# Kernel tuning notes

Measured on AMD Instinct MI355X. Metric: run time of the kernel, lower is better.

## Reference

```python
import jax, jax.numpy as jnp
import numpy as np

WH, WW = 7, 7
N = WH * WW
H = 16          # num_heads
D = 32          # head_dim
NW = 64         # num windows per image (mask.shape[0])


def _relative_position_index(wh, ww):
    coords = np.stack(np.meshgrid(np.arange(wh), np.arange(ww), indexing='ij'))  # (2, wh, ww)
    cf = coords.reshape(2, -1)                                                   # (2, N)
    rel = cf[:, :, None] - cf[:, None, :]                                        # (2, N, N)
    rel = rel.transpose(1, 2, 0).copy()
    rel[:, :, 0] += wh - 1
    rel[:, :, 1] += ww - 1
    rel[:, :, 0] *= 2 * ww - 1
    return rel.sum(-1)  # (N, N) int

REL_IDX = jnp.asarray(_relative_position_index(WH, WW))


def setup_inputs() -> dict:
    key = jax.random.key(0)
    ks = jax.random.split(key, 5)
    B_ = 2048
    dim = H * D
    x = jax.random.normal(ks[0], (B_, N, dim), dtype=jnp.float32)
    mask = jnp.zeros((NW, N, N), dtype=jnp.float32)
    rpb_table = jax.random.normal(ks[1], ((2 * WH - 1) * (2 * WW - 1), H), dtype=jnp.float32) * 0.02
    qkv_w = jax.random.normal(ks[2], (3 * dim, dim), dtype=jnp.float32) * (dim ** -0.5)
    qkv_b = jnp.zeros((3 * dim,), dtype=jnp.float32)
    proj_w = jax.random.normal(ks[3], (dim, dim), dtype=jnp.float32) * (dim ** -0.5)
    proj_b = jnp.zeros((dim,), dtype=jnp.float32)
    return {"x": x, "mask": mask, "rpb_table": rpb_table,
            "qkv_w": qkv_w, "qkv_b": qkv_b, "proj_w": proj_w, "proj_b": proj_b}


def reference(x, mask, rpb_table, qkv_w, qkv_b, proj_w, proj_b):
    B_, n, C = x.shape
    scale = D ** -0.5
    # qkv projection (torch Linear: x @ W^T + b)
    qkv = (x @ qkv_w.T + qkv_b).reshape(B_, n, 3, H, D)
    q = qkv[:, :, 0].transpose(0, 2, 1, 3) * scale  # (B_, H, N, D)
    k = qkv[:, :, 1].transpose(0, 2, 1, 3)
    v = qkv[:, :, 2].transpose(0, 2, 1, 3)
    attn = jnp.einsum('bhnd,bhmd->bhnm', q, k)      # (B_, H, N, N)
    # relative position bias: gather (N*N,) rows from table -> (N, N, H) -> (H, N, N)
    bias = rpb_table[REL_IDX.reshape(-1)].reshape(n, n, H).transpose(2, 0, 1)
    attn = attn + bias[None]
    # shifted-window mask add: (B, nW, H, N, N) + (1, nW, 1, N, N)
    nW = mask.shape[0]
    attn = attn.reshape(B_ // nW, nW, H, n, n) + mask[None, :, None]
    attn = attn.reshape(B_, H, n, n)
    attn = jax.nn.softmax(attn, axis=-1)
    out = jnp.einsum('bhnm,bhmd->bhnd', attn, v)    # (B_, H, N, D)
    out = out.transpose(0, 2, 1, 3).reshape(B_, n, H * D)
    return out @ proj_w.T + proj_b
```

## Files before the change

### kernel.cpp

```cpp
#include <hip/hip_runtime.h>

typedef _Float16 f16;
typedef _Float16 f16x8 __attribute__((ext_vector_type(8)));
typedef _Float16 f16x4 __attribute__((ext_vector_type(4)));
typedef float f32x4 __attribute__((ext_vector_type(4)));

#define NTOK 49
#define NH 16
#define HD 32
#define DIM 512
#define NWIN 64
#define NB 2048
#define MTOT (NB*NTOK)
#define SCALE 0.17677669529663687f
#define VTS 56

__device__ __forceinline__ void gload_lds16(const f16* g, f16* l) {
    __builtin_amdgcn_global_load_lds((const __attribute__((address_space(1))) void*)g,
                                     (__attribute__((address_space(3))) void*)l, 16, 0, 0);
}

__global__ __launch_bounds__(256) void cvt_f32_f16(const float* __restrict__ s,
                                                   f16* __restrict__ d, int n4) {
    int i = blockIdx.x * 256 + threadIdx.x;
    int st = gridDim.x * 256;
    for (; i < n4; i += st) {
        float4 v = ((const float4*)s)[i];
        f16x4 o = { (f16)v.x, (f16)v.y, (f16)v.z, (f16)v.w };
        *(f16x4*)(d + (size_t)i * 4) = o;
    }
}

__global__ __launch_bounds__(256) void build_comb2(const float* __restrict__ rpb,
                                                   const float* __restrict__ mask,
                                                   float* __restrict__ comb2) {
    int idx = blockIdx.x * 256 + threadIdx.x;
    int r4   = idx & 3;
    int tj   = (idx >> 2) & 3;
    int ti   = (idx >> 4) & 3;
    int lane = (idx >> 6) & 63;
    int wh   = idx >> 12;
    int h = wh & 15, w = wh >> 4;
    int g = lane >> 4, c16 = lane & 15;
    int row = ti * 16 + g * 4 + r4;
    int col = tj * 16 + c16;
    float v = 0.f;
    if (row < NTOK && col < NTOK) {
        int ri = row / 7, ci = row - ri * 7;
        int rj = col / 7, cj = col - rj * 7;
        int rel = (ri - rj + 6) * 13 + (ci - cj + 6);
        v = rpb[rel * NH + h] + mask[(w * NTOK + row) * NTOK + col];
    }
    comb2[idx] = v;
}

template<int MODE, int NT>
__global__ __launch_bounds__(256) void gemm_kernel(const f16* __restrict__ A,
                                                   const f16* __restrict__ Bw,
                                                   const float* __restrict__ bias,
                                                   f16* __restrict__ qo,
                                                   f16* __restrict__ ko,
                                                   f16* __restrict__ vto,
                                                   float* __restrict__ outp) {
    __shared__ __align__(16) f16 As[128][64];
    __shared__ __align__(16) f16 Bs[128][64];

    const int tid = threadIdx.x;
    const int lane = tid & 63;
    const int wv = tid >> 6;
    const int wr = wv >> 1, wc = wv & 1;
    const int g = lane >> 4, c16 = lane & 15;

    const int nblk = gridDim.x;
    const int f = blockIdx.x;
    const int work = (f & 7) * (nblk >> 3) + (f >> 3);
    const int m0 = (work / NT) * 128;
    const int n0 = (work % NT) * 128;

    const int sr8 = lane >> 3;
    const int scs = ((lane & 7) ^ sr8) * 8;
    const f16* gA = A + (size_t)(m0 + wv * 32 + sr8) * DIM + scs;
    const f16* gB = Bw + (size_t)(n0 + wv * 32 + sr8) * DIM + scs;

    f32x4 acc[4][4];
#pragma unroll
    for (int i = 0; i < 4; ++i)
#pragma unroll
        for (int j = 0; j < 4; ++j)
            acc[i][j] = (f32x4){0.f, 0.f, 0.f, 0.f};

    const int KS = DIM / 64;
    for (int ks = 0; ks < KS; ++ks) {
        const int k0 = ks * 64;
        __syncthreads();
#pragma unroll
        for (int i = 0; i < 4; ++i) {
            gload_lds16(gA + (size_t)(i * 8) * DIM + k0, &As[wv * 32 + i * 8][0]);
            gload_lds16(gB + (size_t)(i * 8) * DIM + k0, &Bs[wv * 32 + i * 8][0]);
        }
        __syncthreads();
#pragma unroll
        for (int kk = 0; kk < 2; ++kk) {
            f16x8 af[4], bf[4];
#pragma unroll
            for (int t = 0; t < 4; ++t)
                af[t] = *(const f16x8*)&As[wr * 64 + t * 16 + c16][((kk * 4 + g) ^ (c16 & 7)) * 8];
#pragma unroll
            for (int t = 0; t < 4; ++t)
                bf[t] = *(const f16x8*)&Bs[wc * 64 + t * 16 + c16][((kk * 4 + g) ^ (c16 & 7)) * 8];
            __builtin_amdgcn_s_setprio(1);
#pragma unroll
            for (int i = 0; i < 4; ++i)
#pragma unroll
                for (int j = 0; j < 4; ++j)
                    acc[i][j] = __builtin_amdgcn_mfma_f32_16x16x32_f16(af[i], bf[j], acc[i][j], 0, 0, 0);
            __builtin_amdgcn_s_setprio(0);
        }
    }

#pragma unroll
    for (int i = 0; i < 4; ++i)
#pragma unroll
        for (int r = 0; r < 4; ++r) {
            int m = m0 + wr * 64 + i * 16 + g * 4 + r;
            int b = 0, t = 0;
            if (MODE == 0) { b = m / NTOK; t = m - b * NTOK; }
#pragma unroll
            for (int j = 0; j < 4; ++j) {
                int n = n0 + wc * 64 + j * 16 + c16;
                float v = acc[i][j][r] + bias[n];
                if (MODE == 0) {
                    int s = n >> 9;
                    int hh = (n >> 5) & 15;
                    int d = n & 31;
                    int bh = b * NH + hh;
                    if (s == 0)      qo[((size_t)bh * NTOK + t) * HD + d] = (f16)(v * SCALE);
                    else if (s == 1) ko[((size_t)bh * NTOK + t) * HD + d] = (f16)v;
                    else             vto[((size_t)bh * HD + d) * VTS + t] = (f16)v;
                } else {
                    outp[(size_t)m * DIM + n] = v;
                }
            }
        }
}

__global__ __launch_bounds__(256) void attn_kernel(const f16* __restrict__ qw,
                                                   const f16* __restrict__ kw,
                                                   const f16* __restrict__ vt,
                                                   const float* __restrict__ comb2,
                                                   f16* __restrict__ aout) {
    __shared__ __align__(16) f16 Ps[4][64][72];

    const int wv = threadIdx.x >> 6;
    const int l = threadIdx.x & 63;
    const int f = blockIdx.x;
    const int work = (f & 7) * (gridDim.x >> 3) + (f >> 3);
    const int bid = work * 4 + wv;
    const int b = bid >> 4, h = bid & 15;
    const int w = b & (NWIN - 1);
    const int g = l >> 4, c16 = l & 15;
    const size_t qkbase = (size_t)bid * (NTOK * HD);
    const size_t vbase = (size_t)bid * (HD * VTS);

    const f16x8 z8 = {};

    f16x8 qf[4], kf[4];
#pragma unroll
    for (int t = 0; t < 4; ++t) {
        int row = t * 16 + c16;
        f16x8 q = z8, k = z8;
        if (row < NTOK) {
            q = *(const f16x8*)(qw + qkbase + row * HD + g * 8);
            k = *(const f16x8*)(kw + qkbase + row * HD + g * 8);
        }
        qf[t] = q; kf[t] = k;
    }

    const float* cb = comb2 + (((size_t)(w * NH + h) * 64 + l) << 6);
    f32x4 S[4][4];
#pragma unroll
    for (int i = 0; i < 4; ++i)
#pragma unroll
        for (int j = 0; j < 4; ++j)
            S[i][j] = *(const f32x4*)(cb + (i * 4 + j) * 4);
#pragma unroll
    for (int i = 0; i < 4; ++i)
#pragma unroll
        for (int j = 0; j < 4; ++j)
            S[i][j] = __builtin_amdgcn_mfma_f32_16x16x32_f16(qf[i], kf[j], S[i][j], 0, 0, 0);

#pragma unroll
    for (int ti = 0; ti < 4; ++ti)
#pragma unroll
        for (int r = 0; r < 4; ++r) {
            int row = ti * 16 + g * 4 + r;
            float v0 = S[ti][0][r], v1 = S[ti][1][r], v2 = S[ti][2][r];
            float v3 = (c16 == 0) ? S[ti][3][r] : -1e30f;
            float mx = fmaxf(fmaxf(v0, v1), fmaxf(v2, v3));
#pragma unroll
            for (int mk = 1; mk < 16; mk <<= 1) mx = fmaxf(mx, __shfl_xor(mx, mk, 64));
            float p0 = __expf(v0 - mx), p1 = __expf(v1 - mx), p2 = __expf(v2 - mx);
            float p3 = (c16 == 0) ? __expf(v3 - mx) : 0.f;
            float sm = p0 + p1 + p2 + p3;
#pragma unroll
            for (int mk = 1; mk < 16; mk <<= 1) sm += __shfl_xor(sm, mk, 64);
            float inv = 1.f / sm;
            Ps[wv][row][c16]      = (f16)(p0 * inv);
            Ps[wv][row][16 + c16] = (f16)(p1 * inv);
            Ps[wv][row][32 + c16] = (f16)(p2 * inv);
            Ps[wv][row][48 + c16] = (f16)(p3 * inv);
        }
    __syncthreads();

    f32x4 O[4][2];
    const f32x4 zf = (f32x4){0.f, 0.f, 0.f, 0.f};
#pragma unroll
    for (int i = 0; i < 4; ++i) { O[i][0] = zf; O[i][1] = zf; }
#pragma unroll
    for (int c = 0; c < 2; ++c) {
        f16x8 pf[4], vf[2];
#pragma unroll
        for (int ti = 0; ti < 4; ++ti)
            pf[ti] = *(const f16x8*)&Ps[wv][ti * 16 + c16][c * 32 + g * 8];
        int tcol = c * 32 + g * 8;
#pragma unroll
        for (int td = 0; td < 2; ++td) {
            f16x8 vv = z8;
            if (tcol < VTS)
                vv = *(const f16x8*)(vt + vbase + (size_t)(td * 16 + c16) * VTS + tcol);
            vf[td] = vv;
        }
#pragma unroll
        for (int ti = 0; ti < 4; ++ti)
#pragma unroll
            for (int td = 0; td < 2; ++td)
                O[ti][td] = __builtin_amdgcn_mfma_f32_16x16x32_f16(pf[ti], vf[td], O[ti][td], 0, 0, 0);
    }

#pragma unroll
    for (int ti = 0; ti < 4; ++ti)
#pragma unroll
        for (int r = 0; r < 4; ++r) {
            int row = ti * 16 + g * 4 + r;
            if (row < NTOK) {
                size_t ob = ((size_t)(b * NTOK + row)) * DIM + h * HD;
                aout[ob + c16]      = (f16)O[ti][0][r];
                aout[ob + 16 + c16] = (f16)O[ti][1][r];
            }
        }
}

extern "C" void kernel_launch(void* const* d_in, const int* in_sizes, int n_in,
                              void* d_out, int out_size, void* d_ws, size_t ws_size,
                              hipStream_t stream) {
    const float* x      = (const float*)d_in[0];
    const float* mask   = (const float*)d_in[1];
    const float* rpb    = (const float*)d_in[2];
    const float* qkv_w  = (const float*)d_in[3];
    const float* qkv_b  = (const float*)d_in[4];
    const float* proj_w = (const float*)d_in[5];
    const float* proj_b = (const float*)d_in[6];
    float* out = (float*)d_out;

    char* ws = (char*)d_ws;
    size_t o = 0;
    f16* x16   = (f16*)(ws + o); o += (size_t)MTOT * DIM * 2;
    f16* w16   = (f16*)(ws + o); o += (size_t)1536 * 512 * 2;
    f16* pw16  = (f16*)(ws + o); o += (size_t)512 * 512 * 2;
    f16* qws   = (f16*)(ws + o); o += (size_t)NB * NH * NTOK * HD * 2;
    f16* kws   = (f16*)(ws + o); o += (size_t)NB * NH * NTOK * HD * 2;
    f16* vtws  = (f16*)(ws + o); o += (size_t)NB * NH * HD * VTS * 2;
    float* cb2 = (float*)(ws + o);
    f16* aout = x16;

    cvt_f32_f16<<<dim3(2048), dim3(256), 0, stream>>>(x, x16, MTOT * DIM / 4);
    cvt_f32_f16<<<dim3(768), dim3(256), 0, stream>>>(qkv_w, w16, 1536 * 512 / 4);
    cvt_f32_f16<<<dim3(256), dim3(256), 0, stream>>>(proj_w, pw16, 512 * 512 / 4);

    build_comb2<<<dim3(16384), dim3(256), 0, stream>>>(rpb, mask, cb2);

    gemm_kernel<0, 12><<<dim3((MTOT / 128) * 12), dim3(256), 0, stream>>>(
        x16, w16, qkv_b, qws, kws, vtws, nullptr);

    attn_kernel<<<dim3(NB * NH / 4), dim3(256), 0, stream>>>(qws, kws, vtws, cb2, aout);

    gemm_kernel<1, 4><<<dim3((MTOT / 128) * 4), dim3(256), 0, stream>>>(
        aout, pw16, proj_b, nullptr, nullptr, nullptr, out);
}
```

Before: 658.5 us.

## Switch GEMMs to 256x256 tiles with double-buffered LDS prefetch

```diff
diff --git a/kernel.cpp b/kernel.cpp
--- a/kernel.cpp
+++ b/kernel.cpp
@@ -55,79 +55,139 @@
 }
 
 template<int MODE, int NT>
-__global__ __launch_bounds__(256) void gemm_kernel(const f16* __restrict__ A,
-                                                   const f16* __restrict__ Bw,
-                                                   const float* __restrict__ bias,
-                                                   f16* __restrict__ qo,
-                                                   f16* __restrict__ ko,
-                                                   f16* __restrict__ vto,
-                                                   float* __restrict__ outp) {
-    __shared__ __align__(16) f16 As[128][64];
-    __shared__ __align__(16) f16 Bs[128][64];
+__global__ __launch_bounds__(512, 2) void gemm256(const f16* __restrict__ A,
+                                                  const f16* __restrict__ Bw,
+                                                  const float* __restrict__ bias,
+                                                  f16* __restrict__ qo,
+                                                  f16* __restrict__ ko,
+                                                  f16* __restrict__ vto,
+                                                  float* __restrict__ outp) {
+    __shared__ __align__(16) f16 As[2][256][64];
+    __shared__ __align__(16) f16 Bs[2][256][64];
 
     const int tid = threadIdx.x;
     const int lane = tid & 63;
     const int wv = tid >> 6;
-    const int wr = wv >> 1, wc = wv & 1;
+    const int wm = wv >> 2, wn = wv & 3;
     const int g = lane >> 4, c16 = lane & 15;
+    const int sl8 = lane >> 3;
+    const int sc8 = (lane & 7) ^ sl8;
 
     const int nblk = gridDim.x;
     const int f = blockIdx.x;
     const int work = (f & 7) * (nblk >> 3) + (f >> 3);
-    const int m0 = (work / NT) * 128;
-    const int n0 = (work % NT) * 128;
-
-    const int sr8 = lane >> 3;
-    const int scs = ((lane & 7) ^ sr8) * 8;
-    const f16* gA = A + (size_t)(m0 + wv * 32 + sr8) * DIM + scs;
-    const f16* gB = Bw + (size_t)(n0 + wv * 32 + sr8) * DIM + scs;
-
-    f32x4 acc[4][4];
-#pragma unroll
-    for (int i = 0; i < 4; ++i)
+    const int m0 = (work / NT) * 256;
+    const int n0 = (work % NT) * 256;
+
+    const f16* gA0 = A  + (size_t)(m0 + wv * 8 + sl8) * DIM + sc8 * 8;
+    const f16* gB0 = Bw + (size_t)(n0 + wv * 8 + sl8) * DIM + sc8 * 8;
+
+#define STAGE(buf, kof, rd) \
+    gload_lds16(gA0 + (size_t)((rd) * 64) * DIM + (kof), &As[buf][(rd) * 64 + wv * 8][0]); \
+    gload_lds16(gB0 + (size_t)((rd) * 64) * DIM + (kof), &Bs[buf][(rd) * 64 + wv * 8][0]);
+
+#define ARD(half, t2, kk) (*(const f16x8*)&As[pb][wm * 128 + (half) * 64 + (t2) * 16 + c16][((((kk) * 4 + g)) ^ (c16 & 7)) * 8])
+#define BRD(half, j2, kk) (*(const f16x8*)&Bs[pb][wn * 64 + (half) * 32 + (j2) * 16 + c16][((((kk) * 4 + g)) ^ (c16 & 7)) * 8])
+
+    f32x4 acc[8][4];
+#pragma unroll
+    for (int i = 0; i < 8; ++i)
 #pragma unroll
         for (int j = 0; j < 4; ++j)
             acc[i][j] = (f32x4){0.f, 0.f, 0.f, 0.f};
 
-    const int KS = DIM / 64;
-    for (int ks = 0; ks < KS; ++ks) {
-        const int k0 = ks * 64;
-        __syncthreads();
-#pragma unroll
-        for (int i = 0; i < 4; ++i) {
-            gload_lds16(gA + (size_t)(i * 8) * DIM + k0, &As[wv * 32 + i * 8][0]);
-            gload_lds16(gB + (size_t)(i * 8) * DIM + k0, &Bs[wv * 32 + i * 8][0]);
-        }
-        __syncthreads();
-#pragma unroll
-        for (int kk = 0; kk < 2; ++kk) {
-            f16x8 af[4], bf[4];
-#pragma unroll
-            for (int t = 0; t < 4; ++t)
-                af[t] = *(const f16x8*)&As[wr * 64 + t * 16 + c16][((kk * 4 + g) ^ (c16 & 7)) * 8];
-#pragma unroll
-            for (int t = 0; t < 4; ++t)
-                bf[t] = *(const f16x8*)&Bs[wc * 64 + t * 16 + c16][((kk * 4 + g) ^ (c16 & 7)) * 8];
-            __builtin_amdgcn_s_setprio(1);
-#pragma unroll
-            for (int i = 0; i < 4; ++i)
-#pragma unroll
-                for (int j = 0; j < 4; ++j)
-                    acc[i][j] = __builtin_amdgcn_mfma_f32_16x16x32_f16(af[i], bf[j], acc[i][j], 0, 0, 0);
-            __builtin_amdgcn_s_setprio(0);
-        }
-    }
-
-#pragma unroll
-    for (int i = 0; i < 4; ++i)
+#pragma unroll
+    for (int rd = 0; rd < 4; ++rd) { STAGE(0, 0, rd) }
+    asm volatile("s_waitcnt vmcnt(0)" ::: "memory");
+    __builtin_amdgcn_s_barrier();
+
+    const int KT = DIM / 64;
+    for (int t = 0; t < KT; ++t) {
+        const int pb = t & 1, nb = pb ^ 1;
+        const int kn = (t + 1) * 64;
+        const bool hasn = (t + 1 < KT);
+        f16x8 af0[4][2], af1[4][2], bf0[2][2], bf1[2][2];
+
+#pragma unroll
+        for (int t2 = 0; t2 < 4; ++t2)
+#pragma unroll
+            for (int kk = 0; kk < 2; ++kk) af0[t2][kk] = ARD(0, t2, kk);
+#pragma unroll
+        for (int j2 = 0; j2 < 2; ++j2)
+#pragma unroll
+            for (int kk = 0; kk < 2; ++kk) bf0[j2][kk] = BRD(0, j2, kk);
+        if (hasn) { STAGE(nb, kn, 0) STAGE(nb, kn, 1) }
+        __builtin_amdgcn_s_barrier();
+        __builtin_amdgcn_s_setprio(1);
+#pragma unroll
+        for (int t2 = 0; t2 < 4; ++t2)
+#pragma unroll
+            for (int j2 = 0; j2 < 2; ++j2)
+#pragma unroll
+                for (int kk = 0; kk < 2; ++kk)
+                    acc[t2][j2] = __builtin_amdgcn_mfma_f32_16x16x32_f16(af0[t2][kk], bf0[j2][kk], acc[t2][j2], 0, 0, 0);
+        __builtin_amdgcn_s_setprio(0);
+        __builtin_amdgcn_s_barrier();
+
+#pragma unroll
+        for (int j2 = 0; j2 < 2; ++j2)
+#pragma unroll
+            for (int kk = 0; kk < 2; ++kk) bf1[j2][kk] = BRD(1, j2, kk);
+        if (hasn) { STAGE(nb, kn, 2) STAGE(nb, kn, 3) }
+        __builtin_amdgcn_s_barrier();
+        __builtin_amdgcn_s_setprio(1);
+#pragma unroll
+        for (int t2 = 0; t2 < 4; ++t2)
+#pragma unroll
+            for (int j2 = 0; j2 < 2; ++j2)
+#pragma unroll
+                for (int kk = 0; kk < 2; ++kk)
+                    acc[t2][2 + j2] = __builtin_amdgcn_mfma_f32_16x16x32_f16(af0[t2][kk], bf1[j2][kk], acc[t2][2 + j2], 0, 0, 0);
+        __builtin_amdgcn_s_setprio(0);
+        __builtin_amdgcn_s_barrier();
+
+#pragma unroll
+        for (int t2 = 0; t2 < 4; ++t2)
+#pragma unroll
+            for (int kk = 0; kk < 2; ++kk) af1[t2][kk] = ARD(1, t2, kk);
+        __builtin_amdgcn_s_barrier();
+        __builtin_amdgcn_s_setprio(1);
+#pragma unroll
+        for (int t2 = 0; t2 < 4; ++t2)
+#pragma unroll
+            for (int j2 = 0; j2 < 2; ++j2)
+#pragma unroll
+                for (int kk = 0; kk < 2; ++kk)
+                    acc[4 + t2][j2] = __builtin_amdgcn_mfma_f32_16x16x32_f16(af1[t2][kk], bf0[j2][kk], acc[4 + t2][j2], 0, 0, 0);
+        __builtin_amdgcn_s_setprio(0);
+        __builtin_amdgcn_s_barrier();
+
+        __builtin_amdgcn_s_setprio(1);
+#pragma unroll
+        for (int t2 = 0; t2 < 4; ++t2)
+#pragma unroll
+            for (int j2 = 0; j2 < 2; ++j2)
+#pragma unroll
+                for (int kk = 0; kk < 2; ++kk)
+                    acc[4 + t2][2 + j2] = __builtin_amdgcn_mfma_f32_16x16x32_f16(af1[t2][kk], bf1[j2][kk], acc[4 + t2][2 + j2], 0, 0, 0);
+        __builtin_amdgcn_s_setprio(0);
+        if (hasn) asm volatile("s_waitcnt vmcnt(0)" ::: "memory");
+        __builtin_amdgcn_s_barrier();
+    }
+#undef STAGE
+#undef ARD
+#undef BRD
+
+#pragma unroll
+    for (int i = 0; i < 8; ++i)
 #pragma unroll
         for (int r = 0; r < 4; ++r) {
-            int m = m0 + wr * 64 + i * 16 + g * 4 + r;
+            int m = m0 + wm * 128 + i * 16 + g * 4 + r;
             int b = 0, t = 0;
             if (MODE == 0) { b = m / NTOK; t = m - b * NTOK; }
 #pragma unroll
             for (int j = 0; j < 4; ++j) {
-                int n = n0 + wc * 64 + j * 16 + c16;
+                int n = n0 + wn * 64 + j * 16 + c16;
                 float v = acc[i][j][r] + bias[n];
                 if (MODE == 0) {
                     int s = n >> 9;
@@ -279,11 +339,11 @@
 
     build_comb2<<<dim3(16384), dim3(256), 0, stream>>>(rpb, mask, cb2);
 
-    gemm_kernel<0, 12><<<dim3((MTOT / 128) * 12), dim3(256), 0, stream>>>(
+    gemm256<0, 6><<<dim3((MTOT / 256) * 6), dim3(512), 0, stream>>>(
         x16, w16, qkv_b, qws, kws, vtws, nullptr);
 
     attn_kernel<<<dim3(NB * NH / 4), dim3(256), 0, stream>>>(qws, kws, vtws, cb2, aout);
 
-    gemm_kernel<1, 4><<<dim3((MTOT / 128) * 4), dim3(256), 0, stream>>>(
+    gemm256<1, 2><<<dim3((MTOT / 256) * 2), dim3(512), 0, stream>>>(
         aout, pw16, proj_b, nullptr, nullptr, nullptr, out);
 }
```

Result: slower. 692.6 us (+5.2%).

## Triple-buffer GEMM K-loop with async LDS loads and vectorized transposed epilogue

Applied to the files above, without the earlier changes.

```diff
diff --git a/kernel.cpp b/kernel.cpp
--- a/kernel.cpp
+++ b/kernel.cpp
@@ -55,21 +55,22 @@
 }
 
 template<int MODE, int NT>
-__global__ __launch_bounds__(256) void gemm_kernel(const f16* __restrict__ A,
-                                                   const f16* __restrict__ Bw,
-                                                   const float* __restrict__ bias,
-                                                   f16* __restrict__ qo,
-                                                   f16* __restrict__ ko,
-                                                   f16* __restrict__ vto,
-                                                   float* __restrict__ outp) {
-    __shared__ __align__(16) f16 As[128][64];
-    __shared__ __align__(16) f16 Bs[128][64];
+__global__ __launch_bounds__(256, 3) void gemm_kernel(const f16* __restrict__ A,
+                                                      const f16* __restrict__ Bw,
+                                                      const float* __restrict__ bias,
+                                                      f16* __restrict__ qo,
+                                                      f16* __restrict__ ko,
+                                                      f16* __restrict__ vto,
+                                                      float* __restrict__ outp) {
+    __shared__ __align__(16) f16 As[3][128][32];
+    __shared__ __align__(16) f16 Bs[3][128][32];
 
     const int tid = threadIdx.x;
     const int lane = tid & 63;
     const int wv = tid >> 6;
     const int wr = wv >> 1, wc = wv & 1;
     const int g = lane >> 4, c16 = lane & 15;
+    const int rsw = (c16 >> 1) & 3;
 
     const int nblk = gridDim.x;
     const int f = blockIdx.x;
@@ -77,71 +78,94 @@
     const int m0 = (work / NT) * 128;
     const int n0 = (work % NT) * 128;
 
-    const int sr8 = lane >> 3;
-    const int scs = ((lane & 7) ^ sr8) * 8;
-    const f16* gA = A + (size_t)(m0 + wv * 32 + sr8) * DIM + scs;
-    const f16* gB = Bw + (size_t)(n0 + wv * 32 + sr8) * DIM + scs;
+    const int srow = lane >> 2;
+    const int schunk = (lane & 3) ^ ((srow >> 1) & 3);
+    const f16* gA = A  + (size_t)(m0 + wv * 32 + srow) * DIM + schunk * 8;
+    const f16* gB = Bw + (size_t)(n0 + wv * 32 + srow) * DIM + schunk * 8;
+
+#define STAGE(buf, t) do { \
+    gload_lds16(gA + (t) * 32,                     &As[buf][wv * 32][0]);      \
+    gload_lds16(gA + (size_t)16 * DIM + (t) * 32,  &As[buf][wv * 32 + 16][0]); \
+    gload_lds16(gB + (t) * 32,                     &Bs[buf][wv * 32][0]);      \
+    gload_lds16(gB + (size_t)16 * DIM + (t) * 32,  &Bs[buf][wv * 32 + 16][0]); \
+} while (0)
 
     f32x4 acc[4][4];
 #pragma unroll
-    for (int i = 0; i < 4; ++i)
+    for (int j = 0; j < 4; ++j)
+#pragma unroll
+        for (int i = 0; i < 4; ++i)
+            acc[j][i] = (f32x4){0.f, 0.f, 0.f, 0.f};
+
+    STAGE(0, 0);
+    STAGE(1, 1);
+    asm volatile("s_waitcnt vmcnt(4)" ::: "memory");
+    __builtin_amdgcn_s_barrier();
+
+    const int KS = DIM / 32;
+#pragma unroll
+    for (int t = 0; t < KS; ++t) {
+        const int cb = t % 3;
+        if (t + 2 < KS) STAGE((t + 2) % 3, t + 2);
+        f16x8 af[4], bf[4];
+#pragma unroll
+        for (int i = 0; i < 4; ++i)
+            af[i] = *(const f16x8*)&As[cb][wr * 64 + i * 16 + c16][(g ^ rsw) * 8];
 #pragma unroll
         for (int j = 0; j < 4; ++j)
-            acc[i][j] = (f32x4){0.f, 0.f, 0.f, 0.f};
-
-    const int KS = DIM / 64;
-    for (int ks = 0; ks < KS; ++ks) {
-        const int k0 = ks * 64;
-        __syncthreads();
-#pragma unroll
-        for (int i = 0; i < 4; ++i) {
-            gload_lds16(gA + (size_t)(i * 8) * DIM + k0, &As[wv * 32 + i * 8][0]);
-            gload_lds16(gB + (size_t)(i * 8) * DIM + k0, &Bs[wv * 32 + i * 8][0]);
-        }
-        __syncthreads();
-#pragma unroll
-        for (int kk = 0; kk < 2; ++kk) {
-            f16x8 af[4], bf[4];
-#pragma unroll
-            for (int t = 0; t < 4; ++t)
-                af[t] = *(const f16x8*)&As[wr * 64 + t * 16 + c16][((kk * 4 + g) ^ (c16 & 7)) * 8];
-#pragma unroll
-            for (int t = 0; t < 4; ++t)
-                bf[t] = *(const f16x8*)&Bs[wc * 64 + t * 16 + c16][((kk * 4 + g) ^ (c16 & 7)) * 8];
-            __builtin_amdgcn_s_setprio(1);
+            bf[j] = *(const f16x8*)&Bs[cb][wc * 64 + j * 16 + c16][(g ^ rsw) * 8];
+        __builtin_amdgcn_s_setprio(1);
+#pragma unroll
+        for (int j = 0; j < 4; ++j)
 #pragma unroll
             for (int i = 0; i < 4; ++i)
-#pragma unroll
-                for (int j = 0; j < 4; ++j)
-                    acc[i][j] = __builtin_amdgcn_mfma_f32_16x16x32_f16(af[i], bf[j], acc[i][j], 0, 0, 0);
-            __builtin_amdgcn_s_setprio(0);
-        }
-    }
-
-#pragma unroll
-    for (int i = 0; i < 4; ++i)
-#pragma unroll
-        for (int r = 0; r < 4; ++r) {
-            int m = m0 + wr * 64 + i * 16 + g * 4 + r;
-            int b = 0, t = 0;
-            if (MODE == 0) { b = m / NTOK; t = m - b * NTOK; }
-#pragma unroll
-            for (int j = 0; j < 4; ++j) {
-                int n = n0 + wc * 64 + j * 16 + c16;
-                float v = acc[i][j][r] + bias[n];
-                if (MODE == 0) {
-                    int s = n >> 9;
-                    int hh = (n >> 5) & 15;
-                    int d = n & 31;
-                    int bh = b * NH + hh;
-                    if (s == 0)      qo[((size_t)bh * NTOK + t) * HD + d] = (f16)(v * SCALE);
-                    else if (s == 1) ko[((size_t)bh * NTOK + t) * HD + d] = (f16)v;
-                    else             vto[((size_t)bh * HD + d) * VTS + t] = (f16)v;
+                acc[j][i] = __builtin_amdgcn_mfma_f32_16x16x32_f16(bf[j], af[i], acc[j][i], 0, 0, 0);
+        __builtin_amdgcn_s_setprio(0);
+        asm volatile("s_waitcnt lgkmcnt(0)" ::: "memory");
+        __builtin_amdgcn_sched_barrier(0);
+        if (t + 2 < KS) {
+            asm volatile("s_waitcnt vmcnt(4)" ::: "memory");
+        } else if (t + 1 < KS) {
+            asm volatile("s_waitcnt vmcnt(0)" ::: "memory");
+        }
+        if (t + 1 < KS) __builtin_amdgcn_s_barrier();
+    }
+#undef STAGE
+
+#pragma unroll
+    for (int i = 0; i < 4; ++i) {
+        const int m = m0 + wr * 64 + i * 16 + c16;
+        int b = 0, tk = 0;
+        if (MODE == 0) { b = m / NTOK; tk = m - b * NTOK; }
+#pragma unroll
+        for (int j = 0; j < 4; ++j) {
+            const int n = n0 + wc * 64 + j * 16 + g * 4;
+            f32x4 v = acc[j][i];
+            const f32x4 b4 = *(const f32x4*)&bias[n];
+            v += b4;
+            if (MODE == 0) {
+                const int s = n >> 9;
+                const int hh = (n >> 5) & 15;
+                const int d0 = n & 31;
+                const size_t bh = (size_t)(b * NH + hh);
+                if (s == 0) {
+                    f16x4 o = { (f16)(v[0] * SCALE), (f16)(v[1] * SCALE),
+                                (f16)(v[2] * SCALE), (f16)(v[3] * SCALE) };
+                    *(f16x4*)(qo + (bh * NTOK + tk) * HD + d0) = o;
+                } else if (s == 1) {
+                    f16x4 o = { (f16)v[0], (f16)v[1], (f16)v[2], (f16)v[3] };
+                    *(f16x4*)(ko + (bh * NTOK + tk) * HD + d0) = o;
                 } else {
-                    outp[(size_t)m * DIM + n] = v;
+#pragma unroll
+                    for (int r = 0; r < 4; ++r)
+                        vto[(bh * HD + d0 + r) * VTS + tk] = (f16)v[r];
                 }
+            } else {
+                float4 o = { v[0], v[1], v[2], v[3] };
+                *(float4*)(outp + (size_t)m * DIM + n) = o;
             }
         }
+    }
 }
 
 __global__ __launch_bounds__(256) void attn_kernel(const f16* __restrict__ qw,
```

Result: faster. 604.5 us (-8.2%).
